# Kernel optimization log

Hardware: AMD Instinct MI355X
Metric: run time of the kernel (lower is better)

The kernel has to match this reference:

```python
import jax, jax.numpy as jnp
import numpy as np

V, H, W, L, HID = 8, 256, 256, 32, 64
NC, NF = 64, 64
R = 1024


def _grid_sample(img, grid):
    # img [V,C,H,W], grid [V,N,2] with (x,y) in [-1,1]; bilinear, zero padding,
    # align_corners=False (matches torch.nn.functional.grid_sample defaults).
    Vv, C, Hh, Ww = img.shape
    x = (grid[..., 0] + 1.0) * (Ww * 0.5) - 0.5
    y = (grid[..., 1] + 1.0) * (Hh * 0.5) - 0.5
    x0 = jnp.floor(x)
    y0 = jnp.floor(y)
    wx = x - x0
    wy = y - y0
    vidx = jnp.arange(Vv)[:, None]
    def tap(xf, yf):
        valid = (xf >= 0) & (xf <= Ww - 1) & (yf >= 0) & (yf <= Hh - 1)
        xi = jnp.clip(xf, 0, Ww - 1).astype(jnp.int32)
        yi = jnp.clip(yf, 0, Hh - 1).astype(jnp.int32)
        return img[vidx, :, yi, xi] * valid[..., None].astype(img.dtype)  # [V,N,C]
    return (tap(x0, y0) * ((1 - wx) * (1 - wy))[..., None]
            + tap(x0 + 1, y0) * (wx * (1 - wy))[..., None]
            + tap(x0, y0 + 1) * ((1 - wx) * wy)[..., None]
            + tap(x0 + 1, y0 + 1) * (wx * wy)[..., None])  # [V,N,C]


def _sample_pdf(bins, weights, n):
    # NeRF inverse-CDF importance sampling; deterministic midpoint u's.
    w = weights + 1e-5                              # [R, M]
    pdf = w / w.sum(-1, keepdims=True)
    cdf = jnp.concatenate([jnp.zeros_like(pdf[:, :1]), jnp.cumsum(pdf, -1)], -1)  # [R, M+1]
    u = jnp.broadcast_to((jnp.arange(n) + 0.5) / n, (bins.shape[0], n))
    inds = jax.vmap(lambda c, uu: jnp.searchsorted(c, uu, side='right'))(cdf, u)
    below = jnp.clip(inds - 1, 0, cdf.shape[-1] - 1)
    above = jnp.clip(inds, 0, cdf.shape[-1] - 1)
    cdf0 = jnp.take_along_axis(cdf, below, -1)
    cdf1 = jnp.take_along_axis(cdf, above, -1)
    bin0 = jnp.take_along_axis(bins, below, -1)
    bin1 = jnp.take_along_axis(bins, above, -1)
    denom = jnp.where(cdf1 - cdf0 < 1e-5, 1.0, cdf1 - cdf0)
    t = (u - cdf0) / denom
    return bin0 + t * (bin1 - bin0)


def _ibrnet(raw_rgb, feat, src_dirc, ray_dirc, W1, b1, W2, b2, Wd, bd, Wb, bb):
    # IBRNet-style per-view MLP + cross-view pooling for density, softmax
    # blending of source colors for rgb.
    x = jnp.concatenate([raw_rgb, feat, src_dirc,
                         jnp.broadcast_to(ray_dirc[:, None, :], src_dirc.shape)], -1)  # [P,V,3+L+3+3]
    h = jax.nn.relu(x @ W1 + b1)
    h = jax.nn.relu(h @ W2 + b2)                    # [P,V,HID]
    pooled = jnp.concatenate([h.mean(1), h.var(1)], -1)  # [P,2*HID]
    density = pooled @ Wd + bd                      # [P,1]
    blend = jax.nn.softmax((h @ Wb + bb)[..., 0], axis=1)  # [P,V]
    rgb = jnp.einsum('pv,pvc->pc', blend, raw_rgb)  # [P,3]
    return density, rgb


def _composite(depth, density, rgb):
    # NeRF alpha compositing along samples.
    delta = jnp.concatenate([depth[:, 1:] - depth[:, :-1],
                             jnp.full_like(depth[:, :1], 1e10)], -1)
    alpha = 1.0 - jnp.exp(-jax.nn.relu(density) * delta)
    trans = jnp.cumprod(1.0 - alpha + 1e-10, -1)
    trans = jnp.concatenate([jnp.ones_like(trans[:, :1]), trans[:, :-1]], -1)
    w = alpha * trans                               # [R,S]
    return w, (w[..., None] * rgb).sum(1), (w * depth).sum(1), w.sum(1)


def setup_inputs():
    rng = np.random.default_rng(0)

    def look_at(pos):
        pos = np.asarray(pos, np.float64)
        z = -pos / np.linalg.norm(pos)
        up = np.array([0.0, 0.0, 1.0])
        x = np.cross(up, z); x /= np.linalg.norm(x)
        y = np.cross(z, x)
        Rm = np.stack([x, y, z], 0)
        return np.concatenate([Rm, (-Rm @ pos)[:, None]], 1).astype(np.float32)

    ang = np.linspace(0, 2 * np.pi, V, endpoint=False)
    cam_pos = np.stack([3 * np.cos(ang), 3 * np.sin(ang), 0.3 * np.ones(V)], 1)
    E = np.stack([look_at(p) for p in cam_pos], 0)              # [V,3,4]
    f = 300.0
    K = np.broadcast_to(np.array([[f, 0, W / 2], [0, f, H / 2], [0, 0, 1]], np.float32), (V, 3, 3)).copy()

    o = np.array([3.2, 0.1, 0.2], np.float32)
    targets = rng.uniform(-0.2, 0.2, (R, 3)).astype(np.float32)  # points near head center
    d = targets - o
    d /= np.linalg.norm(d, axis=1, keepdims=True)
    dist = float(np.linalg.norm(o))
    near = np.full((R, 1), dist - 0.5, np.float32)
    far = np.full((R, 1), dist + 0.5, np.float32)
    ray = np.concatenate([np.broadcast_to(o, (R, 3)), d, near, far], 1).astype(np.float32)

    inp = {
        'ray': jnp.asarray(ray),
        'source_intrinsic': jnp.asarray(K),
        'source_extrinsic': jnp.asarray(E),
        'source_cam_pos': jnp.asarray(cam_pos.astype(np.float32)),
        'source_shape': jnp.full((V, 2), float(H), jnp.float32),
        'source_mask': jnp.ones((V, 1, H, W), jnp.float32),
        'source_image': jnp.asarray(rng.random((V, 3, H, W), dtype=np.float32)),
        'source_feature': jnp.asarray(rng.standard_normal((V, 2 * L, H, W), dtype=np.float32) * 0.1),
    }
    in_dim = 3 + L + 3 + 3

    def mlp(prefix):
        return {
            prefix + 'W1': jnp.asarray(rng.standard_normal((in_dim, HID), dtype=np.float32) * 0.1),
            prefix + 'b1': jnp.asarray(rng.standard_normal(HID, dtype=np.float32) * 0.01),
            prefix + 'W2': jnp.asarray(rng.standard_normal((HID, HID), dtype=np.float32) * 0.1),
            prefix + 'b2': jnp.asarray(rng.standard_normal(HID, dtype=np.float32) * 0.01),
            prefix + 'Wd': jnp.asarray(rng.standard_normal((2 * HID, 1), dtype=np.float32) * 0.1),
            prefix + 'bd': jnp.asarray(rng.standard_normal(1, dtype=np.float32) * 0.01),
            prefix + 'Wb': jnp.asarray(rng.standard_normal((HID, 1), dtype=np.float32) * 0.1),
            prefix + 'bb': jnp.asarray(rng.standard_normal(1, dtype=np.float32) * 0.01),
        }
    inp.update(mlp('c'))
    inp.update(mlp('f'))
    return inp


def reference(ray, source_intrinsic, source_extrinsic, source_cam_pos, source_shape,
              source_mask, source_image, source_feature,
              cW1, cb1, cW2, cb2, cWd, cbd, cWb, cbb,
              fW1, fb1, fW2, fb2, fWd, fbd, fWb, fbb):
    o, d = ray[:, :3], ray[:, 3:6]
    near, far = ray[:, 6:7], ray[:, 7:8]
    P = jnp.einsum('vij,vjk->vik', source_intrinsic, source_extrinsic)  # [V,3,4]
    wh = source_shape[:, ::-1]                                          # (W,H) per view

    def sample_point(depth):                    # depth [R,S]
        pos = o[:, None, :] + d[:, None, :] * depth[..., None]          # [R,S,3]
        dn = d / jnp.linalg.norm(d, axis=-1, keepdims=True)
        dirc = jnp.broadcast_to(dn[:, None, :], pos.shape)
        pos_h = jnp.concatenate([pos, jnp.ones_like(pos[..., :1])], -1)
        pix = jnp.einsum('rsk,vck->rsvc', pos_h, P)                     # [R,S,V,3]
        pix = pix[..., :2] / (pix[..., 2:3] + 1e-6)
        pix = 2.0 * (pix / wh[None, None]) - 1.0
        return pos, -dirc, pix

    def compute_color(pos, dirc, pix, W1, b1, W2, b2, Wd, bd, Wb, bb, fs, fe):
        Rr, Ss = pix.shape[0], pix.shape[1]
        grid = pix.reshape(Rr * Ss, -1, 2).transpose(1, 0, 2)           # [V,P,2]
        m = _grid_sample(source_mask, grid)[..., 0]                     # [V,P]
        hull = m.sum(0) > (source_mask.shape[0] - 1e-3)                 # visual hull: inside all views
        raw_rgb = _grid_sample(source_image, grid).transpose(1, 0, 2)   # [P,V,3]
        feat = _grid_sample(source_feature, grid)[..., fs:fe].transpose(1, 0, 2)  # [P,V,L]
        pos_f = pos.reshape(-1, 3)
        sd = source_cam_pos[None] - pos_f[:, None]
        sd = sd / jnp.linalg.norm(sd, axis=-1, keepdims=True)
        dens, rgb = _ibrnet(raw_rgb, feat, sd, dirc.reshape(-1, 3), W1, b1, W2, b2, Wd, bd, Wb, bb)
        dens = jnp.where(hull, dens[:, 0], 0.0).reshape(Rr, Ss)
        rgb = jnp.where(hull[:, None], rgb, 0.0).reshape(Rr, Ss, 3)
        return dens, rgb

    # coarse stratified sampling (deterministic bin midpoints)
    t = (jnp.arange(NC) + 0.5) / NC
    c_depth = near + (far - near) * t[None]                             # [R,NC]
    c_pos, c_dir, c_pix = sample_point(c_depth)
    c_dens, c_rgbp = compute_color(c_pos, c_dir, c_pix, cW1, cb1, cW2, cb2, cWd, cbd, cWb, cbb, 0, L)
    c_w, c_rgb, c_dep, c_alp = _composite(c_depth, c_dens, c_rgbp)

    # fine importance sampling from coarse weights
    mids = 0.5 * (c_depth[:, 1:] + c_depth[:, :-1])
    f_depth = _sample_pdf(mids, jax.lax.stop_gradient(c_w[:, 1:-1]), NF)
    full_depth = jnp.sort(jnp.concatenate([c_depth, f_depth], -1), -1)  # [R,NC+NF]
    f_pos, f_dir, f_pix = sample_point(full_depth)
    f_dens, f_rgbp = compute_color(f_pos, f_dir, f_pix, fW1, fb1, fW2, fb2, fWd, fbd, fWb, fbb, L, 2 * L)
    _, f_rgb, f_dep, f_alp = _composite(full_depth, f_dens, f_rgbp)
    return c_rgb, c_dep, c_alp, f_rgb, f_dep, f_alp
```

## Files before the change

kernel.cpp:

```cpp
#include <hip/hip_runtime.h>
#include <hip/hip_bf16.h>
#include <math.h>

#define V_   8
#define H_   256
#define W_   256
#define L_   32
#define HID_ 64
#define NC_  64
#define NF_  64
#define R_   1024
#define IND_ 41
#define HW_  (H_*W_)

typedef __attribute__((ext_vector_type(8)))  short short8v;
typedef __attribute__((ext_vector_type(16))) float f32x16;

__device__ __forceinline__ unsigned int pk2bf(float a, float b) {
    unsigned int ra = (unsigned int)__bfloat16_as_ushort(__float2bfloat16(a));
    unsigned int rb = (unsigned int)__bfloat16_as_ushort(__float2bfloat16(b));
    return ra | (rb << 16);
}

template<int CTRL>
__device__ __forceinline__ float dpp_add(float x) {
    int m = __builtin_amdgcn_mov_dpp(__builtin_bit_cast(int, x), CTRL, 0xF, 0xF, true);
    return x + __builtin_bit_cast(float, m);
}
template<int CTRL>
__device__ __forceinline__ float dpp_max(float x) {
    int m = __builtin_amdgcn_mov_dpp(__builtin_bit_cast(int, x), CTRL, 0xF, 0xF, true);
    return fmaxf(x, __builtin_bit_cast(float, m));
}
__device__ __forceinline__ float vsum8(float x) {
    x = dpp_add<0xB1>(x);
    x = dpp_add<0x4E>(x);
    x += __shfl_xor(x, 4, 64);
    return x;
}
__device__ __forceinline__ float vmax8(float x) {
    x = dpp_max<0xB1>(x);
    x = dpp_max<0x4E>(x);
    x = fmaxf(x, __shfl_xor(x, 4, 64));
    return x;
}
__device__ __forceinline__ float redsum64(float x) {
    #pragma unroll
    for (int off = 32; off >= 1; off >>= 1) x += __shfl_xor(x, off, 64);
    return x;
}
__device__ __forceinline__ float scan_mul64(float x, int lane) {
    #pragma unroll
    for (int off = 1; off < 64; off <<= 1) {
        float y = __shfl_up(x, off, 64);
        x = (lane >= off) ? x * y : x;
    }
    return x;
}
__device__ __forceinline__ float scan_add64(float x, int lane) {
    #pragma unroll
    for (int off = 1; off < 64; off <<= 1) {
        float y = __shfl_up(x, off, 64);
        x = (lane >= off) ? x + y : x;
    }
    return x;
}

__global__ void k_computeP(const float* __restrict__ Km,
                           const float* __restrict__ Em,
                           float* __restrict__ Pm) {
    int t = threadIdx.x;
    if (t >= V_ * 12) return;
    int v = t / 12, e = t - v * 12, row = e >> 2, col = e & 3;
    float acc = 0.f;
    #pragma unroll
    for (int k = 0; k < 3; ++k)
        acc += Km[v * 9 + row * 3 + k] * Em[v * 12 + k * 4 + col];
    Pm[v * 12 + row * 4 + col] = acc;
}

__global__ void k_packMFMA(const float* __restrict__ W1, const float* __restrict__ b1,
                           const float* __restrict__ W2, const float* __restrict__ b2,
                           const float* __restrict__ Wd, const float* __restrict__ Wb,
                           unsigned int* __restrict__ out) {
    int t = blockIdx.x * 256 + threadIdx.x;
    if (t < 1536) {
        int blk = t >> 8, idx = t & 255;
        int mt = blk / 3, kt = blk % 3;
        int l = idx >> 2, rg = idx & 3;
        int hi = l >> 5;
        int j  = 32 * mt + (l & 31);
        int k0 = 16 * kt + 8 * hi + 2 * rg;
        int k1 = k0 + 1;
        float v0 = (k0 < 41) ? W1[k0 * 64 + j] : (k0 == 41 ? b1[j] : 0.f);
        float v1 = (k1 < 41) ? W1[k1 * 64 + j] : (k1 == 41 ? b1[j] : 0.f);
        out[t] = pk2bf(v0, v1);
    } else if (t < 3584) {
        int u = t - 1536;
        int blk = u >> 8, idx = u & 255;
        int l = idx >> 2, rg = idx & 3;
        int hi = l >> 5;
        int j2 = 32 * (blk >> 2) + (l & 31);
        int k0 = 16 * (blk & 3) + 8 * hi + 2 * rg;
        out[t] = pk2bf(W2[k0 * 64 + j2], W2[(k0 + 1) * 64 + j2]);
    } else if (t < 3840) {
        int i = t - 3584;
        int w = i >> 6, mt = (i >> 5) & 1, hi = (i >> 4) & 1, rg = i & 15;
        int j2 = (rg & 3) + 8 * (rg >> 2) + 4 * hi + 32 * mt;
        float v = (w == 0) ? b2[j2] : (w == 1) ? Wb[j2] : (w == 2) ? Wd[j2] : Wd[64 + j2];
        ((float*)out)[t] = v;
    }
}

__global__ __launch_bounds__(256) void k_packB(const float* __restrict__ msk,
                                               const float* __restrict__ img,
                                               const float* __restrict__ fea,
                                               float* __restrict__ pk, int FS) {
    __shared__ unsigned short tile[64][48];
    const int xb = blockIdx.x * 64, y = blockIdx.y, v = blockIdx.z;
    const int t = threadIdx.x;
    const int x = t & 63, cg = t >> 6;
    const size_t px = (size_t)y * W_ + xb + x;
    #pragma unroll
    for (int step = 0; step < 9; ++step) {
        int ch = step * 4 + cg;
        if (ch < 36) {
            float val;
            if (ch == 0)      val = msk[(size_t)v * HW_ + px];
            else if (ch < 4)  val = img[((size_t)(v * 3 + (ch - 1))) * HW_ + px];
            else              val = fea[((size_t)(v * 2 * L_ + FS + (ch - 4))) * HW_ + px];
            tile[x][ch] = __bfloat16_as_ushort(__float2bfloat16(val));
        }
    }
    if (t < 256) { int xi = t >> 2, c = 36 + (t & 3); tile[xi][c] = 0; }
    __syncthreads();
    uint2* dst = (uint2*)(pk + ((size_t)v * HW_ + (size_t)y * W_ + xb) * 20);
    for (int j = t; j < 640; j += 256) {
        int p = j / 10, sl = j % 10;
        dst[j] = *(const uint2*)&tile[p][sl * 4];
    }
}

template <int S, bool FINE>
__global__ __launch_bounds__(256) void k_mlp_mfma(
    const float* __restrict__ ray, const float* __restrict__ Pm,
    const float* __restrict__ cam, const float* __restrict__ shp,
    const float* __restrict__ pk,
    const unsigned int* __restrict__ FR,
    const float* __restrict__ bd, const float* __restrict__ bb,
    const float* __restrict__ deptharr,
    float* __restrict__ odens, float* __restrict__ orgb) {

    __shared__ __align__(16) char smem[40960];
    const int lane = threadIdx.x & 63;
    const int wv   = threadIdx.x >> 6;
    const int hi   = lane >> 5;
    const int l31  = lane & 31;
    char* Xw  = smem + wv * 10240;
    char* H1w = Xw + 6144;

    const int pbase = (blockIdx.x * 4 + wv) * 8;
    const int P0 = pbase + (lane >> 3);
    const int v  = lane & 7;
    const int r  = P0 / S, s = P0 - r * S;

    const float ox = ray[r*8+0], oy = ray[r*8+1], oz = ray[r*8+2];
    const float dx = ray[r*8+3], dy = ray[r*8+4], dz = ray[r*8+5];
    const float nv = ray[r*8+6], fv = ray[r*8+7];

    float depth;
    if (FINE) depth = deptharr[P0];
    else      depth = nv + (fv - nv) * ((s + 0.5f) / (float)S);

    const float px = ox + dx*depth, py = oy + dy*depth, pz = oz + dz*depth;
    const float dn = sqrtf(dx*dx + dy*dy + dz*dz);
    const float rdx = -dx/dn, rdy = -dy/dn, rdz = -dz/dn;

    const float* Pv = Pm + v * 12;
    float q0 = Pv[0]*px + Pv[1]*py + Pv[2]*pz  + Pv[3];
    float q1 = Pv[4]*px + Pv[5]*py + Pv[6]*pz  + Pv[7];
    float q2 = Pv[8]*px + Pv[9]*py + Pv[10]*pz + Pv[11];
    float inv = 1.0f / (q2 + 1e-6f);
    float uu = q0 * inv, ww = q1 * inv;
    float gx = 2.0f * (uu / shp[v*2+1]) - 1.0f;
    float gy = 2.0f * (ww / shp[v*2+0]) - 1.0f;
    float sx = (gx + 1.0f) * ((float)W_ * 0.5f) - 0.5f;
    float sy = (gy + 1.0f) * ((float)H_ * 0.5f) - 0.5f;
    float x0f = floorf(sx), y0f = floorf(sy);
    float fx = sx - x0f, fy = sy - y0f;

    int offp[4]; float wt[4];
    {
        float xs[2] = {x0f, x0f + 1.f}, ys[2] = {y0f, y0f + 1.f};
        float wxs[2] = {1.f - fx, fx},  wys[2] = {1.f - fy, fy};
        #pragma unroll
        for (int t = 0; t < 4; ++t) {
            float xf = xs[t & 1], yf = ys[t >> 1];
            bool val = (xf >= 0.f) && (xf <= (float)(W_-1)) &&
                       (yf >= 0.f) && (yf <= (float)(H_-1));
            int xi = (int)fminf(fmaxf(xf, 0.f), (float)(W_-1));
            int yi = (int)fminf(fmaxf(yf, 0.f), (float)(H_-1));
            offp[t] = yi * W_ + xi;
            wt[t] = wxs[t & 1] * wys[t >> 1] * (val ? 1.f : 0.f);
        }
    }

    float vals[40];
    #pragma unroll
    for (int i = 0; i < 40; ++i) vals[i] = 0.f;
    #pragma unroll
    for (int t = 0; t < 4; ++t) {
        const uint4* fp = (const uint4*)pk + ((size_t)v * HW_ + offp[t]) * 5;
        float wtt = wt[t];
        #pragma unroll
        for (int s5 = 0; s5 < 5; ++s5) {
            uint4 q = fp[s5];
            unsigned int dw[4] = {q.x, q.y, q.z, q.w};
            #pragma unroll
            for (int e = 0; e < 4; ++e) {
                int i = s5 * 8 + e * 2;
                vals[i]   += wtt * __uint_as_float(dw[e] << 16);
                vals[i+1] += wtt * __uint_as_float(dw[e] & 0xFFFF0000u);
            }
        }
    }
    float msample = vals[0];
    float rv0 = vals[1], rv1 = vals[2], rv2 = vals[3];
    float sdx = cam[v*3+0]-px, sdy = cam[v*3+1]-py, sdz = cam[v*3+2]-pz;
    float snv = sqrtf(sdx*sdx + sdy*sdy + sdz*sdz);
    sdx /= snv; sdy /= snv; sdz /= snv;

    float xx[42];
    xx[0] = rv0; xx[1] = rv1; xx[2] = rv2;
    #pragma unroll
    for (int k = 0; k < 32; ++k) xx[3+k] = vals[4+k];
    xx[35] = sdx; xx[36] = sdy; xx[37] = sdz;
    xx[38] = rdx; xx[39] = rdy; xx[40] = rdz;
    xx[41] = 1.0f;

    {
        unsigned int d[24];
        #pragma unroll
        for (int i = 0; i < 21; ++i) d[i] = pk2bf(xx[2*i], xx[2*i+1]);
        d[21] = 0u; d[22] = 0u; d[23] = 0u;
        #pragma unroll
        for (int o = 0; o < 6; ++o)
            *(uint4*)(Xw + o * 1024 + lane * 16) =
                make_uint4(d[o*4], d[o*4+1], d[o*4+2], d[o*4+3]);
    }

    short8v aw1[6];
    #pragma unroll
    for (int i = 0; i < 6; ++i)
        aw1[i] = __builtin_bit_cast(short8v, ((const uint4*)FR)[i * 64 + lane]);
    const float4* PL4 = (const float4*)(FR + 3584);
    const float bdv = bd[0], bbv = bb[0];

    float hs = vsum8(msample);
    float hssw  = __shfl_xor(hs, 32, 64);
    float rv0sw = __shfl_xor(rv0, 32, 64);
    float rv1sw = __shfl_xor(rv1, 32, 64);
    float rv2sw = __shfl_xor(rv2, 32, 64);

    #pragma unroll
    for (int nt = 0; nt < 2; ++nt) {
        const int n = nt * 32 + l31;
        f32x16 acc1[2];
        #pragma unroll
        for (int mt = 0; mt < 2; ++mt)
            #pragma unroll
            for (int q = 0; q < 16; ++q) acc1[mt][q] = 0.f;
        #pragma unroll
        for (int kt = 0; kt < 3; ++kt) {
            uint4 bu = *(const uint4*)(Xw + (2*kt + hi) * 1024 + n * 16);
            short8v b = __builtin_bit_cast(short8v, bu);
            acc1[0] = __builtin_amdgcn_mfma_f32_32x32x16_bf16(aw1[kt],     b, acc1[0], 0, 0, 0);
            acc1[1] = __builtin_amdgcn_mfma_f32_32x32x16_bf16(aw1[3 + kt], b, acc1[1], 0, 0, 0);
        }
        #pragma unroll
        for (int mt = 0; mt < 2; ++mt)
            #pragma unroll
            for (int q = 0; q < 4; ++q) {
                unsigned int w0 = pk2bf(fmaxf(acc1[mt][4*q+0], 0.f),
                                        fmaxf(acc1[mt][4*q+1], 0.f));
                unsigned int w1 = pk2bf(fmaxf(acc1[mt][4*q+2], 0.f),
                                        fmaxf(acc1[mt][4*q+3], 0.f));
                *(uint2*)(H1w + (q + 4*mt) * 512 + l31 * 16 + hi * 8) = make_uint2(w0, w1);
            }
        short8v aw2[8];
        #pragma unroll
        for (int i = 0; i < 8; ++i)
            aw2[i] = __builtin_bit_cast(short8v, ((const uint4*)(FR + 1536))[i * 64 + lane]);
        f32x16 acc2[2];
        #pragma unroll
        for (int mt = 0; mt < 2; ++mt)
            #pragma unroll
            for (int q4 = 0; q4 < 4; ++q4) {
                float4 c = PL4[(mt*2 + hi)*4 + q4];
                acc2[mt][4*q4+0] = c.x; acc2[mt][4*q4+1] = c.y;
                acc2[mt][4*q4+2] = c.z; acc2[mt][4*q4+3] = c.w;
            }
        #pragma unroll
        for (int kt = 0; kt < 4; ++kt) {
            uint4 bu = *(const uint4*)(H1w + (2*kt + hi) * 512 + l31 * 16);
            short8v b = __builtin_bit_cast(short8v, bu);
            acc2[0] = __builtin_amdgcn_mfma_f32_32x32x16_bf16(aw2[kt],     b, acc2[0], 0, 0, 0);
            acc2[1] = __builtin_amdgcn_mfma_f32_32x32x16_bf16(aw2[4 + kt], b, acc2[1], 0, 0, 0);
        }

        float lgp = 0.f, dacc = 0.f, cacc = 0.f;
        #pragma unroll
        for (int mt = 0; mt < 2; ++mt)
            #pragma unroll
            for (int q4 = 0; q4 < 4; ++q4) {
                float4 wb4 = PL4[16 + (mt*2 + hi)*4 + q4];
                float4 wd4 = PL4[32 + (mt*2 + hi)*4 + q4];
                float4 w24 = PL4[48 + (mt*2 + hi)*4 + q4];
                #pragma unroll
                for (int e = 0; e < 4; ++e) {
                    float hv = fmaxf(acc2[mt][4*q4+e], 0.f);
                    float wbv = (e==0)?wb4.x:(e==1)?wb4.y:(e==2)?wb4.z:wb4.w;
                    float wdv = (e==0)?wd4.x:(e==1)?wd4.y:(e==2)?wd4.z:wd4.w;
                    float w2v = (e==0)?w24.x:(e==1)?w24.y:(e==2)?w24.z:w24.w;
                    lgp  += hv * wbv;
                    dacc += hv * wdv + hv * hv * w2v;
                    float sj = vsum8(hv);
                    cacc += sj * sj * w2v;
                }
            }
        float lg = lgp + __shfl_xor(lgp, 32, 64) + bbv;
        dacc += __shfl_xor(dacc, 32, 64);
        dacc  = vsum8(dacc);
        cacc += __shfl_xor(cacc, 32, 64);
        float density = dacc * 0.125f - cacc * (1.0f / 64.0f) + bdv;

        float mx = vmax8(lg);
        float e  = expf(lg - mx);
        float es = vsum8(e);
        float r0c = (hi == nt) ? rv0 : rv0sw;
        float r1c = (hi == nt) ? rv1 : rv1sw;
        float r2c = (hi == nt) ? rv2 : rv2sw;
        float br  = vsum8(e * r0c);
        float bg  = vsum8(e * r1c);
        float bbl = vsum8(e * r2c);
        float hn  = (nt == 0) ? hs : hssw;
        bool hull = hn > ((float)V_ - 0.001f);

        if ((lane & 0x27) == 0) {
            int PP = pbase + 4 * nt + (lane >> 3);
            float is = 1.0f / es;
            odens[PP]      = hull ? density  : 0.f;
            orgb[PP*3 + 0] = hull ? br  * is : 0.f;
            orgb[PP*3 + 1] = hull ? bg  * is : 0.f;
            orgb[PP*3 + 2] = hull ? bbl * is : 0.f;
        }
    }
}

template <int S, int FS, bool FINE>
__global__ __launch_bounds__(256, 2) void k_mlp_fb(
    const float* __restrict__ ray, const float* __restrict__ Pm,
    const float* __restrict__ cam, const float* __restrict__ shp,
    const float* __restrict__ msk, const float* __restrict__ img,
    const float* __restrict__ fea,
    const float* __restrict__ W1, const float* __restrict__ b1,
    const float* __restrict__ W2, const float* __restrict__ b2,
    const float* __restrict__ Wd, const float* __restrict__ bd,
    const float* __restrict__ Wb, const float* __restrict__ bb,
    const float* __restrict__ deptharr,
    float* __restrict__ odens, float* __restrict__ orgb) {

    const int tid = blockIdx.x * 256 + threadIdx.x;
    const int v   = tid & 7;
    const int P   = tid >> 3;
    const int r   = P / S, s = P - r * S;

    const float ox = ray[r*8+0], oy = ray[r*8+1], oz = ray[r*8+2];
    const float dx = ray[r*8+3], dy = ray[r*8+4], dz = ray[r*8+5];
    const float nv = ray[r*8+6], fv = ray[r*8+7];
    float depth;
    if (FINE) depth = deptharr[P];
    else      depth = nv + (fv - nv) * ((s + 0.5f) / (float)S);
    const float px = ox + dx*depth, py = oy + dy*depth, pz = oz + dz*depth;
    const float dn = sqrtf(dx*dx + dy*dy + dz*dz);
    const float rdx = -dx/dn, rdy = -dy/dn, rdz = -dz/dn;
    const float* Pv = Pm + v * 12;
    float q0 = Pv[0]*px + Pv[1]*py + Pv[2]*pz  + Pv[3];
    float q1 = Pv[4]*px + Pv[5]*py + Pv[6]*pz  + Pv[7];
    float q2 = Pv[8]*px + Pv[9]*py + Pv[10]*pz + Pv[11];
    float inv = 1.0f / (q2 + 1e-6f);
    float uu = q0 * inv, ww = q1 * inv;
    float gx = 2.0f * (uu / shp[v*2+1]) - 1.0f;
    float gy = 2.0f * (ww / shp[v*2+0]) - 1.0f;
    float sx = (gx + 1.0f) * ((float)W_ * 0.5f) - 0.5f;
    float sy = (gy + 1.0f) * ((float)H_ * 0.5f) - 0.5f;
    float x0f = floorf(sx), y0f = floorf(sy);
    float fx = sx - x0f, fy = sy - y0f;
    int offp[4]; float wt[4];
    {
        float xs[2] = {x0f, x0f + 1.f}, ys[2] = {y0f, y0f + 1.f};
        float wxs[2] = {1.f - fx, fx},  wys[2] = {1.f - fy, fy};
        #pragma unroll
        for (int t = 0; t < 4; ++t) {
            float xf = xs[t & 1], yf = ys[t >> 1];
            bool val = (xf >= 0.f) && (xf <= (float)(W_-1)) &&
                       (yf >= 0.f) && (yf <= (float)(H_-1));
            int xi = (int)fminf(fmaxf(xf, 0.f), (float)(W_-1));
            int yi = (int)fminf(fmaxf(yf, 0.f), (float)(H_-1));
            offp[t] = yi * W_ + xi;
            wt[t] = wxs[t & 1] * wys[t >> 1] * (val ? 1.f : 0.f);
        }
    }
    const float* mb = msk + v * HW_;
    float msample = wt[0]*mb[offp[0]] + wt[1]*mb[offp[1]]
                  + wt[2]*mb[offp[2]] + wt[3]*mb[offp[3]];
    float rv0 = 0.f, rv1 = 0.f, rv2 = 0.f;
    {
        const float* ib = img + (v * 3) * HW_;
        #pragma unroll
        for (int t = 0; t < 4; ++t) {
            rv0 += wt[t] * ib[offp[t]];
            rv1 += wt[t] * ib[HW_ + offp[t]];
            rv2 += wt[t] * ib[2 * HW_ + offp[t]];
        }
    }
    float sdx = cam[v*3+0]-px, sdy = cam[v*3+1]-py, sdz = cam[v*3+2]-pz;
    float snv = sqrtf(sdx*sdx + sdy*sdy + sdz*sdz);
    sdx /= snv; sdy /= snv; sdz /= snv;
    float xx[IND_];
    xx[0] = rv0; xx[1] = rv1; xx[2] = rv2;
    #pragma unroll
    for (int k = 0; k < 32; ++k) {
        const float* fb = fea + (size_t)(v * (2*L_) + FS + k) * HW_;
        xx[3+k] = wt[0]*fb[offp[0]] + wt[1]*fb[offp[1]]
                + wt[2]*fb[offp[2]] + wt[3]*fb[offp[3]];
    }
    xx[35] = sdx; xx[36] = sdy; xx[37] = sdz;
    xx[38] = rdx; xx[39] = rdy; xx[40] = rdz;
    float h1[HID_];
    #pragma unroll
    for (int j = 0; j < HID_; ++j) {
        float a0 = 0.f;
        #pragma unroll
        for (int k = 0; k < IND_; ++k) a0 += xx[k] * W1[k * HID_ + j];
        h1[j] = fmaxf(b1[j] + a0, 0.f);
    }
    float lg = bb[0];
    float A = 0.f, B = 0.f, C = 0.f;
    #pragma unroll 1
    for (int j = 0; j < HID_; j += 4) {
        float hh[4];
        #pragma unroll
        for (int jj = 0; jj < 4; ++jj) {
            float a0 = 0.f;
            #pragma unroll
            for (int k = 0; k < HID_; ++k) a0 += h1[k] * W2[k * HID_ + (j + jj)];
            hh[jj] = fmaxf(b2[j + jj] + a0, 0.f);
        }
        #pragma unroll
        for (int jj = 0; jj < 4; ++jj) {
            float h = hh[jj];
            lg += h * Wb[j + jj];
            A  += h * Wd[j + jj];
            B  += h * h * Wd[HID_ + j + jj];
            float sj = vsum8(h);
            C  += sj * sj * Wd[HID_ + j + jj];
        }
    }
    A = vsum8(A); B = vsum8(B);
    float density = A * 0.125f + B * 0.125f - C * (1.0f / 64.0f) + bd[0];
    float hsv = vsum8(msample);
    bool hull = hsv > ((float)V_ - 0.001f);
    float mx = vmax8(lg);
    float e = expf(lg - mx);
    float es = vsum8(e);
    float br  = vsum8(e * rv0);
    float bg  = vsum8(e * rv1);
    float bbl = vsum8(e * rv2);
    if (v == 0) {
        float is = 1.0f / es;
        odens[P]      = hull ? density  : 0.f;
        orgb[P*3 + 0] = hull ? br  * is : 0.f;
        orgb[P*3 + 1] = hull ? bg  * is : 0.f;
        orgb[P*3 + 2] = hull ? bbl * is : 0.f;
    }
}

__global__ __launch_bounds__(256) void k_comp_coarse(const float* __restrict__ ray,
                                                     const float* __restrict__ dens,
                                                     const float* __restrict__ rgb,
                                                     float* __restrict__ out,
                                                     float* __restrict__ fulld) {
    __shared__ float cdfS[4][64];
    __shared__ float fdS[4][64];
    const int wv = threadIdx.x >> 6, lane = threadIdx.x & 63;
    const int r = blockIdx.x * 4 + wv;
    const float nv = ray[r*8+6], fv = ray[r*8+7];
    const int s = lane;

    float d0 = nv + (fv - nv) * ((s + 0.5f) / NC_);
    float d1 = nv + (fv - nv) * ((s + 1.5f) / NC_);
    float delta = (s == NC_-1) ? 1e10f : (d1 - d0);
    float a = 1.f - expf(-fmaxf(dens[r*NC_ + s], 0.f) * delta);
    float qv = 1.f - a + 1e-10f;
    float inc = scan_mul64(qv, lane);
    float trans = __shfl_up(inc, 1, 64);
    if (lane == 0) trans = 1.f;
    float w = a * trans;

    float g0 = rgb[(r*NC_+s)*3+0], g1 = rgb[(r*NC_+s)*3+1], g2 = rgb[(r*NC_+s)*3+2];
    float c0 = redsum64(w * g0);
    float c1 = redsum64(w * g1);
    float c2 = redsum64(w * g2);
    float cd = redsum64(w * d0);
    float ca = redsum64(w);
    if (lane == 0) {
        out[r*3+0] = c0; out[r*3+1] = c1; out[r*3+2] = c2;
        out[3072 + r] = cd;
        out[4096 + r] = ca;
    }

    float pw = (s >= 1 && s <= 62) ? (w + 1e-5f) : 0.f;
    float tot = redsum64(pw);
    float p = pw / tot;
    float ic = scan_add64(p, lane);
    cdfS[wv][lane] = ic;
    __syncthreads();

    float u = (lane + 0.5f) / NF_;
    int lo = 0, hi = 63;
    while (lo < hi) {
        int mid = (lo + hi) >> 1;
        if (cdfS[wv][mid] <= u) lo = mid + 1; else hi = mid;
    }
    int below = lo - 1;
    int above = (lo > 62) ? 62 : lo;
    float cA = cdfS[wv][below], cB = cdfS[wv][above];
    float b0 = nv + (fv - nv) * ((below + 1.0f) / NC_);
    float b1 = nv + (fv - nv) * ((above + 1.0f) / NC_);
    float dnm = cB - cA;
    dnm = (dnm < 1e-5f) ? 1.f : dnm;
    float fdv = b0 + (u - cA) / dnm * (b1 - b0);
    fdS[wv][lane] = fdv;
    __syncthreads();

    lo = 0; hi = 64;
    while (lo < hi) {
        int mid = (lo + hi) >> 1;
        if (fdS[wv][mid] < d0) lo = mid + 1; else hi = mid;
    }
    fulld[r*128 + s + lo] = d0;

    lo = 0; hi = 64;
    while (lo < hi) {
        int mid = (lo + hi) >> 1;
        float daj = nv + (fv - nv) * ((mid + 0.5f) / NC_);
        if (daj <= fdv) lo = mid + 1; else hi = mid;
    }
    fulld[r*128 + lane + lo] = fdv;
}

__global__ __launch_bounds__(256) void k_comp_fine(const float* __restrict__ fulld,
                                                   const float* __restrict__ dens,
                                                   const float* __restrict__ rgb,
                                                   float* __restrict__ out) {
    const int wv = threadIdx.x >> 6, lane = threadIdx.x & 63;
    const int r = blockIdx.x * 4 + wv;
    const int S = NC_ + NF_;
    const float* fl = fulld + r * S;
    const int s0 = 2 * lane, s1 = 2 * lane + 1;

    float f0 = fl[s0], f1 = fl[s1];
    float nx = __shfl_down(f0, 1, 64);
    float dl0 = f1 - f0;
    float dl1 = (lane == 63) ? 1e10f : (nx - f1);
    float a0 = 1.f - expf(-fmaxf(dens[r*S + s0], 0.f) * dl0);
    float a1 = 1.f - expf(-fmaxf(dens[r*S + s1], 0.f) * dl1);
    float q0 = 1.f - a0 + 1e-10f, q1 = 1.f - a1 + 1e-10f;
    float inc = scan_mul64(q0 * q1, lane);
    float E = __shfl_up(inc, 1, 64);
    if (lane == 0) E = 1.f;
    float w0 = a0 * E, w1 = a1 * (E * q0);

    float g00 = rgb[(r*S+s0)*3+0], g01 = rgb[(r*S+s0)*3+1], g02 = rgb[(r*S+s0)*3+2];
    float g10 = rgb[(r*S+s1)*3+0], g11 = rgb[(r*S+s1)*3+1], g12 = rgb[(r*S+s1)*3+2];
    float c0 = redsum64(w0*g00 + w1*g10);
    float c1 = redsum64(w0*g01 + w1*g11);
    float c2 = redsum64(w0*g02 + w1*g12);
    float cd = redsum64(w0*f0 + w1*f1);
    float ca = redsum64(w0 + w1);
    if (lane == 0) {
        out[5120 + r*3+0] = c0; out[5120 + r*3+1] = c1; out[5120 + r*3+2] = c2;
        out[8192 + r] = cd;
        out[9216 + r] = ca;
    }
}

extern "C" void kernel_launch(void* const* d_in, const int* in_sizes, int n_in,
                              void* d_out, int out_size, void* d_ws, size_t ws_size,
                              hipStream_t stream) {
    const float* ray = (const float*)d_in[0];
    const float* Kin = (const float*)d_in[1];
    const float* Ein = (const float*)d_in[2];
    const float* cam = (const float*)d_in[3];
    const float* shp = (const float*)d_in[4];
    const float* msk = (const float*)d_in[5];
    const float* img = (const float*)d_in[6];
    const float* fea = (const float*)d_in[7];
    const float* cw[8]; for (int i = 0; i < 8; ++i) cw[i] = (const float*)d_in[8+i];
    const float* fw[8]; for (int i = 0; i < 8; ++i) fw[i] = (const float*)d_in[16+i];

    float* ws    = (float*)d_ws;
    float* Pm    = ws;
    unsigned int* FRc = (unsigned int*)(Pm + 96);
    unsigned int* FRf = FRc + 4096;
    float* cdens = (float*)(FRf + 4096);
    float* crgb  = cdens + R_ * NC_;
    float* fulld = crgb + R_ * NC_ * 3;
    float* fdens = fulld + R_ * (NC_+NF_);
    float* frgb  = fdens + R_ * (NC_+NF_);
    float* pk    = frgb + R_ * (NC_+NF_) * 3;

    size_t base_floats = (size_t)(pk - ws);
    size_t need = (base_floats + (size_t)V_ * HW_ * 20 + 64) * sizeof(float);
    bool packed = (ws_size >= need);

    float* outp  = (float*)d_out;

    k_computeP<<<1, 96, 0, stream>>>(Kin, Ein, Pm);

    if (packed) {
        k_packMFMA<<<15, 256, 0, stream>>>(cw[0], cw[1], cw[2], cw[3], cw[4], cw[6], FRc);
        k_packMFMA<<<15, 256, 0, stream>>>(fw[0], fw[1], fw[2], fw[3], fw[4], fw[6], FRf);
        k_packB<<<dim3(W_/64, H_, V_), 256, 0, stream>>>(msk, img, fea, pk, 0);

        k_mlp_mfma<NC_, false><<<R_ * NC_ / 32, 256, 0, stream>>>(
            ray, Pm, cam, shp, pk, FRc, cw[5], cw[7],
            nullptr, cdens, crgb);

        k_comp_coarse<<<R_ / 4, 256, 0, stream>>>(ray, cdens, crgb, outp, fulld);

        k_packB<<<dim3(W_/64, H_, V_), 256, 0, stream>>>(msk, img, fea, pk, L_);

        k_mlp_mfma<NC_ + NF_, true><<<R_ * (NC_+NF_) / 32, 256, 0, stream>>>(
            ray, Pm, cam, shp, pk, FRf, fw[5], fw[7],
            fulld, fdens, frgb);

        k_comp_fine<<<R_ / 4, 256, 0, stream>>>(fulld, fdens, frgb, outp);
    } else {
        k_mlp_fb<NC_, 0, false><<<R_ * NC_ * 8 / 256, 256, 0, stream>>>(
            ray, Pm, cam, shp, msk, img, fea,
            cw[0], cw[1], cw[2], cw[3], cw[4], cw[5], cw[6], cw[7],
            nullptr, cdens, crgb);

        k_comp_coarse<<<R_ / 4, 256, 0, stream>>>(ray, cdens, crgb, outp, fulld);

        k_mlp_fb<NC_ + NF_, L_, true><<<R_ * (NC_+NF_) * 8 / 256, 256, 0, stream>>>(
            ray, Pm, cam, shp, msk, img, fea,
            fw[0], fw[1], fw[2], fw[3], fw[4], fw[5], fw[6], fw[7],
            fulld, fdens, frgb);

        k_comp_fine<<<R_ / 4, 256, 0, stream>>>(fulld, fdens, frgb, outp);
    }
}
```

Measured before the change: 197.4 us.

## Merge init kernels and pack coarse+fine features in a single pass

Fuses the projection-matrix and both weight-packing kernels into one launch, and replaces the two per-stage feature packing kernels with one that writes coarse and fine channel groups interleaved per pixel (80 bf16 per pixel). The MLP kernels select their half with a template offset. This removes two launches and a second read of mask and image, but doubles the packed buffer stride, which may hurt gather locality for each MLP's bilinear taps. It also swaps the xor-4 shuffle for a ds_swizzle in the 8-lane reductions.

```diff
diff --git a/kernel.cpp b/kernel.cpp
--- a/kernel.cpp
+++ b/kernel.cpp
@@ -32,16 +32,20 @@
     int m = __builtin_amdgcn_mov_dpp(__builtin_bit_cast(int, x), CTRL, 0xF, 0xF, true);
     return fmaxf(x, __builtin_bit_cast(float, m));
 }
+__device__ __forceinline__ float swz_xor4(float x) {
+    int m = __builtin_amdgcn_ds_swizzle(__builtin_bit_cast(int, x), 0x101F);
+    return __builtin_bit_cast(float, m);
+}
 __device__ __forceinline__ float vsum8(float x) {
     x = dpp_add<0xB1>(x);
     x = dpp_add<0x4E>(x);
-    x += __shfl_xor(x, 4, 64);
+    x += swz_xor4(x);
     return x;
 }
 __device__ __forceinline__ float vmax8(float x) {
     x = dpp_max<0xB1>(x);
     x = dpp_max<0x4E>(x);
-    x = fmaxf(x, __shfl_xor(x, 4, 64));
+    x = fmaxf(x, swz_xor4(x));
     return x;
 }
 __device__ __forceinline__ float redsum64(float x) {
@@ -66,24 +70,11 @@
     return x;
 }
 
-__global__ void k_computeP(const float* __restrict__ Km,
-                           const float* __restrict__ Em,
-                           float* __restrict__ Pm) {
-    int t = threadIdx.x;
-    if (t >= V_ * 12) return;
-    int v = t / 12, e = t - v * 12, row = e >> 2, col = e & 3;
-    float acc = 0.f;
-    #pragma unroll
-    for (int k = 0; k < 3; ++k)
-        acc += Km[v * 9 + row * 3 + k] * Em[v * 12 + k * 4 + col];
-    Pm[v * 12 + row * 4 + col] = acc;
-}
-
-__global__ void k_packMFMA(const float* __restrict__ W1, const float* __restrict__ b1,
-                           const float* __restrict__ W2, const float* __restrict__ b2,
-                           const float* __restrict__ Wd, const float* __restrict__ Wb,
-                           unsigned int* __restrict__ out) {
-    int t = blockIdx.x * 256 + threadIdx.x;
+__device__ __forceinline__ void packMFMA_body(
+    int t, const float* __restrict__ W1, const float* __restrict__ b1,
+    const float* __restrict__ W2, const float* __restrict__ b2,
+    const float* __restrict__ Wd, const float* __restrict__ Wb,
+    unsigned int* __restrict__ out) {
     if (t < 1536) {
         int blk = t >> 8, idx = t & 255;
         int mt = blk / 3, kt = blk % 3;
@@ -112,36 +103,70 @@
     }
 }
 
-__global__ __launch_bounds__(256) void k_packB(const float* __restrict__ msk,
-                                               const float* __restrict__ img,
-                                               const float* __restrict__ fea,
-                                               float* __restrict__ pk, int FS) {
-    __shared__ unsigned short tile[64][48];
+__global__ __launch_bounds__(256) void k_init(
+    const float* __restrict__ Km, const float* __restrict__ Em, float* __restrict__ Pm,
+    const float* __restrict__ cW1, const float* __restrict__ cb1,
+    const float* __restrict__ cW2, const float* __restrict__ cb2,
+    const float* __restrict__ cWd, const float* __restrict__ cWb,
+    unsigned int* __restrict__ FRc,
+    const float* __restrict__ fW1, const float* __restrict__ fb1,
+    const float* __restrict__ fW2, const float* __restrict__ fb2,
+    const float* __restrict__ fWd, const float* __restrict__ fWb,
+    unsigned int* __restrict__ FRf) {
+    const int bid = blockIdx.x, tid = threadIdx.x;
+    if (bid == 0) {
+        if (tid >= V_ * 12) return;
+        int v = tid / 12, e = tid - v * 12, row = e >> 2, col = e & 3;
+        float acc = 0.f;
+        #pragma unroll
+        for (int k = 0; k < 3; ++k)
+            acc += Km[v * 9 + row * 3 + k] * Em[v * 12 + k * 4 + col];
+        Pm[v * 12 + row * 4 + col] = acc;
+    } else if (bid <= 15) {
+        packMFMA_body((bid - 1) * 256 + tid, cW1, cb1, cW2, cb2, cWd, cWb, FRc);
+    } else if (bid <= 30) {
+        packMFMA_body((bid - 16) * 256 + tid, fW1, fb1, fW2, fb2, fWd, fWb, FRf);
+    }
+}
+
+__global__ __launch_bounds__(256) void k_packB2(const float* __restrict__ msk,
+                                                const float* __restrict__ img,
+                                                const float* __restrict__ fea,
+                                                float* __restrict__ pk) {
+    __shared__ unsigned short tile[64][80];
     const int xb = blockIdx.x * 64, y = blockIdx.y, v = blockIdx.z;
     const int t = threadIdx.x;
     const int x = t & 63, cg = t >> 6;
     const size_t px = (size_t)y * W_ + xb + x;
     #pragma unroll
-    for (int step = 0; step < 9; ++step) {
+    for (int step = 0; step < 17; ++step) {
         int ch = step * 4 + cg;
-        if (ch < 36) {
+        if (ch < 68) {
             float val;
             if (ch == 0)      val = msk[(size_t)v * HW_ + px];
             else if (ch < 4)  val = img[((size_t)(v * 3 + (ch - 1))) * HW_ + px];
-            else              val = fea[((size_t)(v * 2 * L_ + FS + (ch - 4))) * HW_ + px];
-            tile[x][ch] = __bfloat16_as_ushort(__float2bfloat16(val));
-        }
-    }
-    if (t < 256) { int xi = t >> 2, c = 36 + (t & 3); tile[xi][c] = 0; }
+            else              val = fea[((size_t)(v * 2 * L_ + (ch - 4))) * HW_ + px];
+            unsigned short bf = __bfloat16_as_ushort(__float2bfloat16(val));
+            if (ch == 0)      { tile[x][0] = bf; tile[x][40] = bf; }
+            else if (ch < 4)  { tile[x][ch] = bf; tile[x][40 + ch] = bf; }
+            else if (ch < 36) { tile[x][ch] = bf; }
+            else              { tile[x][ch + 8] = bf; }
+        }
+    }
+    if (t < 256) {
+        int xi = t >> 2, c = t & 3;
+        tile[xi][36 + c] = 0;
+        tile[xi][76 + c] = 0;
+    }
     __syncthreads();
-    uint2* dst = (uint2*)(pk + ((size_t)v * HW_ + (size_t)y * W_ + xb) * 20);
-    for (int j = t; j < 640; j += 256) {
-        int p = j / 10, sl = j % 10;
+    uint2* dst = (uint2*)(pk + ((size_t)v * HW_ + (size_t)y * W_ + xb) * 40);
+    for (int j = t; j < 1280; j += 256) {
+        int p = j / 20, sl = j % 20;
         dst[j] = *(const uint2*)&tile[p][sl * 4];
     }
 }
 
-template <int S, bool FINE>
+template <int S, bool FINE, int GOFF>
 __global__ __launch_bounds__(256) void k_mlp_mfma(
     const float* __restrict__ ray, const float* __restrict__ Pm,
     const float* __restrict__ cam, const float* __restrict__ shp,
@@ -210,7 +235,7 @@
     for (int i = 0; i < 40; ++i) vals[i] = 0.f;
     #pragma unroll
     for (int t = 0; t < 4; ++t) {
-        const uint4* fp = (const uint4*)pk + ((size_t)v * HW_ + offp[t]) * 5;
+        const uint4* fp = (const uint4*)pk + ((size_t)v * HW_ + offp[t]) * 10 + GOFF;
         float wtt = wt[t];
         #pragma unroll
         for (int s5 = 0; s5 < 5; ++s5) {
@@ -622,32 +647,32 @@
     float* pk    = frgb + R_ * (NC_+NF_) * 3;
 
     size_t base_floats = (size_t)(pk - ws);
-    size_t need = (base_floats + (size_t)V_ * HW_ * 20 + 64) * sizeof(float);
+    size_t need = (base_floats + (size_t)V_ * HW_ * 40 + 64) * sizeof(float);
     bool packed = (ws_size >= need);
 
     float* outp  = (float*)d_out;
 
-    k_computeP<<<1, 96, 0, stream>>>(Kin, Ein, Pm);
-
     if (packed) {
-        k_packMFMA<<<15, 256, 0, stream>>>(cw[0], cw[1], cw[2], cw[3], cw[4], cw[6], FRc);
-        k_packMFMA<<<15, 256, 0, stream>>>(fw[0], fw[1], fw[2], fw[3], fw[4], fw[6], FRf);
-        k_packB<<<dim3(W_/64, H_, V_), 256, 0, stream>>>(msk, img, fea, pk, 0);
-
-        k_mlp_mfma<NC_, false><<<R_ * NC_ / 32, 256, 0, stream>>>(
+        k_init<<<31, 256, 0, stream>>>(Kin, Ein, Pm,
+            cw[0], cw[1], cw[2], cw[3], cw[4], cw[6], FRc,
+            fw[0], fw[1], fw[2], fw[3], fw[4], fw[6], FRf);
+        k_packB2<<<dim3(W_/64, H_, V_), 256, 0, stream>>>(msk, img, fea, pk);
+
+        k_mlp_mfma<NC_, false, 0><<<R_ * NC_ / 32, 256, 0, stream>>>(
             ray, Pm, cam, shp, pk, FRc, cw[5], cw[7],
             nullptr, cdens, crgb);
 
         k_comp_coarse<<<R_ / 4, 256, 0, stream>>>(ray, cdens, crgb, outp, fulld);
 
-        k_packB<<<dim3(W_/64, H_, V_), 256, 0, stream>>>(msk, img, fea, pk, L_);
-
-        k_mlp_mfma<NC_ + NF_, true><<<R_ * (NC_+NF_) / 32, 256, 0, stream>>>(
+        k_mlp_mfma<NC_ + NF_, true, 5><<<R_ * (NC_+NF_) / 32, 256, 0, stream>>>(
             ray, Pm, cam, shp, pk, FRf, fw[5], fw[7],
             fulld, fdens, frgb);
 
         k_comp_fine<<<R_ / 4, 256, 0, stream>>>(fulld, fdens, frgb, outp);
     } else {
+        k_init<<<1, 256, 0, stream>>>(Kin, Ein, Pm,
+            cw[0], cw[1], cw[2], cw[3], cw[4], cw[6], FRc,
+            fw[0], fw[1], fw[2], fw[3], fw[4], fw[6], FRf);
         k_mlp_fb<NC_, 0, false><<<R_ * NC_ * 8 / 256, 256, 0, stream>>>(
             ray, Pm, cam, shp, msk, img, fea,
             cw[0], cw[1], cw[2], cw[3], cw[4], cw[5], cw[6], cw[7],
```

After: 193.0 us. 2.2% less time.
